# Kernel optimization log

Measured on AMD Instinct MI355X. Metric: run time of the kernel, lower is better.

The kernel has to match this reference:

```python
import jax, jax.numpy as jnp
import numpy as np
import math

B, T, D = 2, 2048, 1024
H, DH = 16, 64          # num_heads, head_dim
DFF = 4096              # 4*d_model
EPS = 1e-5


def _layernorm(x, g, b):
    m = jnp.mean(x, axis=-1, keepdims=True)
    v = jnp.mean(jnp.square(x - m), axis=-1, keepdims=True)
    return (x - m) * jax.lax.rsqrt(v + EPS) * g + b


def setup_inputs() -> dict:
    key = jax.random.key(0)
    ks = jax.random.split(key, 6)
    s = 0.02
    return {
        "x": jax.random.normal(ks[0], (B, T, D), dtype=jnp.float32),
        "ln1_g": jnp.ones((D,), jnp.float32), "ln1_b": jnp.zeros((D,), jnp.float32),
        "ln2_g": jnp.ones((D,), jnp.float32), "ln2_b": jnp.zeros((D,), jnp.float32),
        "w_qkv": jax.random.normal(ks[1], (3 * D, D), jnp.float32) * s,
        "b_qkv": jnp.zeros((3 * D,), jnp.float32),
        "w_out": jax.random.normal(ks[2], (D, D), jnp.float32) * s,
        "b_out": jnp.zeros((D,), jnp.float32),
        "w1": jax.random.normal(ks[3], (DFF, D), jnp.float32) * s,
        "b1": jnp.zeros((DFF,), jnp.float32),
        "w2": jax.random.normal(ks[4], (D, DFF), jnp.float32) * s,
        "b2": jnp.zeros((D,), jnp.float32),
    }


def reference(x, ln1_g, ln1_b, ln2_g, ln2_b, w_qkv, b_qkv, w_out, b_out, w1, b1, w2, b2):
    # --- attention sublayer (Pre-LN) ---
    h = _layernorm(x, ln1_g, ln1_b)                       # [B,T,D]
    qkv = h @ w_qkv.T + b_qkv                             # [B,T,3D]
    qkv = qkv.reshape(B, T, 3, H, DH).transpose(2, 0, 3, 1, 4)  # [3,B,H,T,DH]
    q, k, v = qkv[0], qkv[1], qkv[2]
    scores = jnp.einsum('bhqd,bhkd->bhqk', q, k) / math.sqrt(DH)  # [B,H,T,T]
    causal = jnp.tril(jnp.ones((T, T), dtype=bool))
    scores = jnp.where(causal, scores, -jnp.inf)
    weights = jax.nn.softmax(scores, axis=-1)
    attn = jnp.einsum('bhqk,bhkd->bhqd', weights, v)      # [B,H,T,DH]
    attn = attn.transpose(0, 2, 1, 3).reshape(B, T, D)
    x = x + (attn @ w_out.T + b_out)

    # --- FFN sublayer (Pre-LN, exact GELU) ---
    h2 = _layernorm(x, ln2_g, ln2_b)
    ff = jax.nn.gelu(h2 @ w1.T + b1, approximate=False) @ w2.T + b2
    return x + ff
```

## Files before the change

kernel.cpp:

```cpp
#include <hip/hip_runtime.h>
#include <hip/hip_bf16.h>
#include <cmath>

typedef __bf16 bf16x8 __attribute__((ext_vector_type(8)));
typedef float  f32x4  __attribute__((ext_vector_type(4)));

#define LDS_AS __attribute__((address_space(3)))
#define GLB_AS __attribute__((address_space(1)))

__device__ __forceinline__ void gll16(const void* g, void* l) {
    __builtin_amdgcn_global_load_lds((const GLB_AS unsigned int*)g,
                                     (LDS_AS unsigned int*)l, 16, 0, 0);
}

__device__ __forceinline__ f32x4 mfma16(bf16x8 a, bf16x8 b, f32x4 c) {
    return __builtin_amdgcn_mfma_f32_16x16x32_bf16(a, b, c, 0, 0, 0);
}

__device__ __forceinline__ unsigned short f2bf(float f) {
    __hip_bfloat16 b = __float2bfloat16(f);
    return *reinterpret_cast<unsigned short*>(&b);
}

__device__ __forceinline__ bf16x8 swzfrag(const __hip_bfloat16* __restrict__ lds,
                                          int row, int cb)
{
    const int addr = row * 128 + (cb ^ ((row & 7) << 4));
    return *(const bf16x8*)((const char*)lds + addr);
}

__device__ __forceinline__ void stage64x128B(const char* __restrict__ base, int pitch,
                                             char* __restrict__ lds, int t)
{
#pragma unroll
    for (int i = 0; i < 2; ++i) {
        const int d   = i * 4096 + t * 16;
        const int row = d >> 7;
        const int x   = d & 127;
        const int gx  = x ^ ((row & 7) << 4);
        gll16(base + (size_t)row * pitch + gx, lds + d);
    }
}

__device__ __forceinline__ void stage128x128B(const char* __restrict__ base, int pitch,
                                              char* __restrict__ lds, int t)
{
#pragma unroll
    for (int i = 0; i < 4; ++i) {
        const int d   = i * 4096 + t * 16;
        const int row = d >> 7;
        const int x   = d & 127;
        const int gx  = x ^ ((row & 7) << 4);
        gll16(base + (size_t)row * pitch + gx, lds + d);
    }
}

#define TB   2
#define TT   2048
#define TD   1024
#define TH   16
#define TDH  64
#define TDFF 4096
#define TM   4096

__global__ __launch_bounds__(256)
void cvt_kernel(const float* __restrict__ src, __hip_bfloat16* __restrict__ dst, int n4)
{
    int i = blockIdx.x * 256 + threadIdx.x;
    if (i >= n4) return;
    float4 v = ((const float4*)src)[i];
    ushort4 o;
    o.x = f2bf(v.x); o.y = f2bf(v.y); o.z = f2bf(v.z); o.w = f2bf(v.w);
    ((ushort4*)dst)[i] = o;
}

__global__ __launch_bounds__(256)
void ln_kernel(const float* __restrict__ x, const float* __restrict__ g,
               const float* __restrict__ b, __hip_bfloat16* __restrict__ out)
{
    const int row = blockIdx.x;
    const int t = threadIdx.x;
    const float4 v = *(const float4*)(x + (size_t)row * TD + t * 4);
    float s  = v.x + v.y + v.z + v.w;
    float ss = v.x*v.x + v.y*v.y + v.z*v.z + v.w*v.w;
#pragma unroll
    for (int d = 1; d < 64; d <<= 1) { s += __shfl_xor(s, d); ss += __shfl_xor(ss, d); }
    __shared__ float red[8];
    const int wv = t >> 6, lane = t & 63;
    if (lane == 0) { red[wv] = s; red[4 + wv] = ss; }
    __syncthreads();
    s  = red[0] + red[1] + red[2] + red[3];
    ss = red[4] + red[5] + red[6] + red[7];
    const float mean = s * (1.0f / TD);
    const float var  = ss * (1.0f / TD) - mean * mean;
    const float rstd = rsqrtf(var + 1e-5f);
    const float4 gv = *(const float4*)(g + t * 4);
    const float4 bv = *(const float4*)(b + t * 4);
    ushort4 o;
    o.x = f2bf((v.x - mean) * rstd * gv.x + bv.x);
    o.y = f2bf((v.y - mean) * rstd * gv.y + bv.y);
    o.z = f2bf((v.z - mean) * rstd * gv.z + bv.z);
    o.w = f2bf((v.w - mean) * rstd * gv.w + bv.w);
    *(ushort4*)(out + (size_t)row * TD + t * 4) = o;
}

template<int EPI>
__global__ __launch_bounds__(256)
void gemm_bt(const __hip_bfloat16* __restrict__ A, const __hip_bfloat16* __restrict__ Bw,
             const float* __restrict__ bias, const float* __restrict__ resid,
             float* __restrict__ outf, __hip_bfloat16* __restrict__ outb,
             __hip_bfloat16* __restrict__ qb, __hip_bfloat16* __restrict__ kb,
             __hip_bfloat16* __restrict__ vtb,
             int M, int N, int K)
{
    __shared__ __hip_bfloat16 ldsA[2][128 * 64];
    __shared__ __hip_bfloat16 ldsB[2][128 * 64];
    const int t = threadIdx.x;
    const int lane = t & 63, wv = t >> 6;
    const int wr = wv >> 1, wc = wv & 1;
    const int l15 = lane & 15, lg = lane >> 4;
    const int bn = blockIdx.x, bm = blockIdx.y;
    f32x4 acc[4][4] = {};

    const char* Ab = (const char*)(A  + (size_t)bm * 128 * K);
    const char* Bb = (const char*)(Bw + (size_t)bn * 128 * K);
    const int pitch = K * 2;

    const int nt = K >> 6;
    stage128x128B(Ab, pitch, (char*)ldsA[0], t);
    stage128x128B(Bb, pitch, (char*)ldsB[0], t);
    __syncthreads();

    int cur = 0;
    for (int it = 0; it < nt; ++it) {
        if (it + 1 < nt) {
            const size_t koff = (size_t)(it + 1) * 128;
            stage128x128B(Ab + koff, pitch, (char*)ldsA[cur ^ 1], t);
            stage128x128B(Bb + koff, pitch, (char*)ldsB[cur ^ 1], t);
        }
        bf16x8 af[4][2], bfr[4][2];
#pragma unroll
        for (int mf = 0; mf < 4; ++mf)
#pragma unroll
            for (int kk = 0; kk < 2; ++kk)
                af[mf][kk] = swzfrag(ldsA[cur], wr * 64 + mf * 16 + l15, kk * 64 + lg * 16);
#pragma unroll
        for (int nf = 0; nf < 4; ++nf)
#pragma unroll
            for (int kk = 0; kk < 2; ++kk)
                bfr[nf][kk] = swzfrag(ldsB[cur], wc * 64 + nf * 16 + l15, kk * 64 + lg * 16);
        __builtin_amdgcn_s_setprio(1);
#pragma unroll
        for (int mf = 0; mf < 4; ++mf)
#pragma unroll
            for (int nf = 0; nf < 4; ++nf) {
                acc[mf][nf] = mfma16(af[mf][0], bfr[nf][0], acc[mf][nf]);
                acc[mf][nf] = mfma16(af[mf][1], bfr[nf][1], acc[mf][nf]);
            }
        __builtin_amdgcn_s_setprio(0);
        __syncthreads();
        cur ^= 1;
    }

#pragma unroll
    for (int mf = 0; mf < 4; ++mf) {
#pragma unroll
        for (int nf = 0; nf < 4; ++nf) {
#pragma unroll
            for (int r = 0; r < 4; ++r) {
                const int mg = bm * 128 + wr * 64 + mf * 16 + lg * 4 + r;
                const int ng = bn * 128 + wc * 64 + nf * 16 + l15;
                float v = acc[mf][nf][r] + bias[ng];
                if constexpr (EPI == 1) {
                    const size_t o = (size_t)mg * N + ng;
                    outf[o] = v + resid[o];
                } else if constexpr (EPI == 2) {
                    const float ge = 0.5f * v * (1.0f + erff(v * 0.70710678118654752f));
                    outb[(size_t)mg * N + ng] = __float2bfloat16(ge);
                } else {
                    const int which = ng >> 10;
                    const int hh = (ng >> 6) & 15;
                    const int dh = ng & 63;
                    const int bb = mg >> 11;
                    const int tt = mg & 2047;
                    const int bhid = bb * TH + hh;
                    const __hip_bfloat16 bv = __float2bfloat16(v);
                    if (which == 0)      qb[((size_t)bhid * TT + tt) * TDH + dh] = bv;
                    else if (which == 1) kb[((size_t)bhid * TT + tt) * TDH + dh] = bv;
                    else                 vtb[((size_t)bhid * TDH + dh) * TT + tt] = bv;
                }
            }
        }
    }
}

__global__ __launch_bounds__(256)
void flash_kernel(const __hip_bfloat16* __restrict__ q, const __hip_bfloat16* __restrict__ k,
                  const __hip_bfloat16* __restrict__ vt, __hip_bfloat16* __restrict__ attn)
{
    const int L  = blockIdx.y * gridDim.x + blockIdx.x;
    const int cu = L & 255;
    const int s  = L >> 8;
    const int q0 = cu & 31;
    const int qt = (s & 1) ? (31 - q0) : q0;
    const int bh = s * 8 + (cu >> 5);

    const int t = threadIdx.x;
    const int w = t >> 6, lane = t & 63;
    const int l15 = lane & 15, lg = lane >> 4;
    const int qrow0 = qt * 64 + w * 16;
    const __hip_bfloat16* Qb = q  + (size_t)bh * TT * TDH;
    const __hip_bfloat16* Kb = k  + (size_t)bh * TT * TDH;
    const __hip_bfloat16* Vb = vt + (size_t)bh * TDH * TT;

    __shared__ __hip_bfloat16 kt[2][64 * 64];
    __shared__ __hip_bfloat16 vtt[2][64 * 64];
    __shared__ __hip_bfloat16 plds[4][16 * 64];

    bf16x8 qa[2];
#pragma unroll
    for (int c = 0; c < 2; ++c)
        qa[c] = *(const bf16x8*)(Qb + (size_t)(qrow0 + l15) * TDH + c * 32 + lg * 8);

    f32x4 o[4] = {};
    float mrun = -INFINITY, lrun = 0.0f;

    const int nt = qt + 1;
    int cur = 0;
    stage64x128B((const char*)Kb, 128, (char*)kt[0], t);
    stage64x128B((const char*)Vb, TT * 2, (char*)vtt[0], t);
    __syncthreads();

    for (int it = 0; it < nt; ++it) {
        const int kv0 = it * 64;
        if (it + 1 < nt) {
            stage64x128B((const char*)Kb + (size_t)(kv0 + 64) * 128, 128, (char*)kt[cur ^ 1], t);
            stage64x128B((const char*)Vb + (size_t)(kv0 + 64) * 2, TT * 2, (char*)vtt[cur ^ 1], t);
        }
        f32x4 sc[4] = {};
#pragma unroll
        for (int j = 0; j < 4; ++j) {
            const bf16x8 kb0 = swzfrag(kt[cur], j * 16 + l15, lg * 16);
            const bf16x8 kb1 = swzfrag(kt[cur], j * 16 + l15, 64 + lg * 16);
            sc[j] = mfma16(kb0, qa[0], sc[j]);
            sc[j] = mfma16(kb1, qa[1], sc[j]);
        }
        if (it == nt - 1) {
            const int qg = qrow0 + l15;
#pragma unroll
            for (int j = 0; j < 4; ++j)
#pragma unroll
                for (int r = 0; r < 4; ++r) {
                    const int kvg = kv0 + j * 16 + lg * 4 + r;
                    sc[j][r] = (kvg <= qg) ? sc[j][r] * 0.125f : -INFINITY;
                }
        } else {
#pragma unroll
            for (int j = 0; j < 4; ++j)
#pragma unroll
                for (int r = 0; r < 4; ++r) sc[j][r] *= 0.125f;
        }
        float pm;
        {
            float m0 = fmaxf(fmaxf(sc[0][0], sc[0][1]), fmaxf(sc[0][2], sc[0][3]));
            float m1 = fmaxf(fmaxf(sc[1][0], sc[1][1]), fmaxf(sc[1][2], sc[1][3]));
            float m2 = fmaxf(fmaxf(sc[2][0], sc[2][1]), fmaxf(sc[2][2], sc[2][3]));
            float m3 = fmaxf(fmaxf(sc[3][0], sc[3][1]), fmaxf(sc[3][2], sc[3][3]));
            pm = fmaxf(fmaxf(m0, m1), fmaxf(m2, m3));
        }
        pm = fmaxf(pm, __shfl_xor(pm, 16));
        pm = fmaxf(pm, __shfl_xor(pm, 32));

        const float mn = fmaxf(mrun, pm);
        const float alpha = __expf(mrun - mn);
        mrun = mn;
        f32x4 p[4];
        float rs = 0.0f;
#pragma unroll
        for (int j = 0; j < 4; ++j) {
            float a = 0.0f;
#pragma unroll
            for (int r = 0; r < 4; ++r) { p[j][r] = __expf(sc[j][r] - mn); a += p[j][r]; }
            rs += a;
        }
        rs += __shfl_xor(rs, 16);
        rs += __shfl_xor(rs, 32);
        lrun = lrun * alpha + rs;
#pragma unroll
        for (int nf = 0; nf < 4; ++nf)
#pragma unroll
            for (int r = 0; r < 4; ++r) o[nf][r] *= alpha;
        {
            __hip_bfloat16* pw = plds[w];
#pragma unroll
            for (int j = 0; j < 4; ++j) {
                ushort4 pk;
                pk.x = f2bf(p[j][0]); pk.y = f2bf(p[j][1]);
                pk.z = f2bf(p[j][2]); pk.w = f2bf(p[j][3]);
                const int cb = j * 32 + lg * 8;
                *(ushort4*)((char*)pw + l15 * 128 + (cb ^ ((l15 & 7) << 4))) = pk;
            }
        }
        asm volatile("s_waitcnt lgkmcnt(0)" ::: "memory");
        __builtin_amdgcn_sched_barrier(0);
        bf16x8 pb[2];
#pragma unroll
        for (int c = 0; c < 2; ++c)
            pb[c] = swzfrag(plds[w], l15, c * 64 + lg * 16);
#pragma unroll
        for (int nf = 0; nf < 4; ++nf) {
            const bf16x8 vb0 = swzfrag(vtt[cur], nf * 16 + l15, lg * 16);
            const bf16x8 vb1 = swzfrag(vtt[cur], nf * 16 + l15, 64 + lg * 16);
            o[nf] = mfma16(vb0, pb[0], o[nf]);
            o[nf] = mfma16(vb1, pb[1], o[nf]);
        }
        __syncthreads();
        cur ^= 1;
    }

    const int bb = bh >> 4, hh = bh & 15;
    const float inv = 1.0f / lrun;
    const int tt = qrow0 + l15;
#pragma unroll
    for (int nf = 0; nf < 4; ++nf) {
        const int d0 = nf * 16 + lg * 4;
        ushort4 st;
        st.x = f2bf(o[nf][0] * inv);
        st.y = f2bf(o[nf][1] * inv);
        st.z = f2bf(o[nf][2] * inv);
        st.w = f2bf(o[nf][3] * inv);
        *(ushort4*)(attn + ((size_t)(bb * TT + tt)) * TD + hh * TDH + d0) = st;
    }
}

extern "C" void kernel_launch(void* const* d_in, const int* in_sizes, int n_in,
                              void* d_out, int out_size, void* d_ws, size_t ws_size,
                              hipStream_t stream)
{
    const float* x     = (const float*)d_in[0];
    const float* ln1_g = (const float*)d_in[1];
    const float* ln1_b = (const float*)d_in[2];
    const float* ln2_g = (const float*)d_in[3];
    const float* ln2_b = (const float*)d_in[4];
    const float* w_qkv = (const float*)d_in[5];
    const float* b_qkv = (const float*)d_in[6];
    const float* w_out = (const float*)d_in[7];
    const float* b_out = (const float*)d_in[8];
    const float* w1    = (const float*)d_in[9];
    const float* b1    = (const float*)d_in[10];
    const float* w2    = (const float*)d_in[11];
    const float* b2    = (const float*)d_in[12];

    char* ws = (char*)d_ws;
    __hip_bfloat16* wqkv_bf = (__hip_bfloat16*)(ws + 0);
    __hip_bfloat16* wout_bf = (__hip_bfloat16*)(ws + 6291456);
    __hip_bfloat16* w1_bf   = (__hip_bfloat16*)(ws + 8388608);
    __hip_bfloat16* w2_bf   = (__hip_bfloat16*)(ws + 16777216);
    float*          x2      = (float*)(ws + 25165824);
    __hip_bfloat16* hbuf    = (__hip_bfloat16*)(ws + 41943040);
    __hip_bfloat16* qbuf    = (__hip_bfloat16*)(ws + 50331648);
    __hip_bfloat16* kbuf    = (__hip_bfloat16*)(ws + 58720256);
    __hip_bfloat16* vtbuf   = (__hip_bfloat16*)(ws + 67108864);
    __hip_bfloat16* attnbuf = (__hip_bfloat16*)(ws + 75497472);
    __hip_bfloat16* ff1     = (__hip_bfloat16*)(ws + 50331648);

    cvt_kernel<<<3072, 256, 0, stream>>>(w_qkv, wqkv_bf, 3 * TD * TD / 4);
    cvt_kernel<<<1024, 256, 0, stream>>>(w_out, wout_bf, TD * TD / 4);
    cvt_kernel<<<4096, 256, 0, stream>>>(w1, w1_bf, TDFF * TD / 4);
    cvt_kernel<<<4096, 256, 0, stream>>>(w2, w2_bf, TD * TDFF / 4);

    ln_kernel<<<TM, 256, 0, stream>>>(x, ln1_g, ln1_b, hbuf);
    gemm_bt<0><<<dim3(24, 32), 256, 0, stream>>>(hbuf, wqkv_bf, b_qkv, nullptr,
                                                 nullptr, nullptr, qbuf, kbuf, vtbuf,
                                                 TM, 3 * TD, TD);
    flash_kernel<<<dim3(32, 32), 256, 0, stream>>>(qbuf, kbuf, vtbuf, attnbuf);
    gemm_bt<1><<<dim3(8, 32), 256, 0, stream>>>(attnbuf, wout_bf, b_out, x,
                                                x2, nullptr, nullptr, nullptr, nullptr,
                                                TM, TD, TD);
    ln_kernel<<<TM, 256, 0, stream>>>(x2, ln2_g, ln2_b, hbuf);
    gemm_bt<2><<<dim3(32, 32), 256, 0, stream>>>(hbuf, w1_bf, b1, nullptr,
                                                 nullptr, ff1, nullptr, nullptr, nullptr,
                                                 TM, TDFF, TD);
    gemm_bt<1><<<dim3(8, 32), 256, 0, stream>>>(ff1, w2_bf, b2, x2,
                                                (float*)d_out, nullptr, nullptr, nullptr, nullptr,
                                                TM, TD, TDFF);
}
```

Before: 292.6 us.

## Use split-K with atomic accumulation for output and FFN-down projections

The two GEMMs with N=1024 are split four ways along K, and each split accumulates its partial product into the fp32 output with atomicAdd. A separate kernel first writes residual plus bias into the output buffer. This raises the block count from 256 to 1024 so more compute units stay busy. In exchange it adds atomic read-modify-write traffic, an extra elementwise pass, and a nondeterministic summation order.

```diff
diff --git a/kernel.cpp b/kernel.cpp
--- a/kernel.cpp
+++ b/kernel.cpp
@@ -72,6 +72,19 @@
     ushort4 o;
     o.x = f2bf(v.x); o.y = f2bf(v.y); o.z = f2bf(v.z); o.w = f2bf(v.w);
     ((ushort4*)dst)[i] = o;
+}
+
+__global__ __launch_bounds__(256)
+void addbias_kernel(const float* __restrict__ resid, const float* __restrict__ bias,
+                    float* __restrict__ out)
+{
+    const int row = blockIdx.x;
+    const int t = threadIdx.x;
+    const float4 r = *(const float4*)(resid + (size_t)row * TD + t * 4);
+    const float4 b = *(const float4*)(bias + t * 4);
+    float4 o;
+    o.x = r.x + b.x; o.y = r.y + b.y; o.z = r.z + b.z; o.w = r.w + b.w;
+    *(float4*)(out + (size_t)row * TD + t * 4) = o;
 }
 
 __global__ __launch_bounds__(256)
@@ -111,7 +124,7 @@
              float* __restrict__ outf, __hip_bfloat16* __restrict__ outb,
              __hip_bfloat16* __restrict__ qb, __hip_bfloat16* __restrict__ kb,
              __hip_bfloat16* __restrict__ vtb,
-             int M, int N, int K)
+             int M, int N, int K, int Kpitch)
 {
     __shared__ __hip_bfloat16 ldsA[2][128 * 64];
     __shared__ __hip_bfloat16 ldsB[2][128 * 64];
@@ -119,12 +132,12 @@
     const int lane = t & 63, wv = t >> 6;
     const int wr = wv >> 1, wc = wv & 1;
     const int l15 = lane & 15, lg = lane >> 4;
-    const int bn = blockIdx.x, bm = blockIdx.y;
+    const int bn = blockIdx.x, bm = blockIdx.y, kz = blockIdx.z;
     f32x4 acc[4][4] = {};
 
-    const char* Ab = (const char*)(A  + (size_t)bm * 128 * K);
-    const char* Bb = (const char*)(Bw + (size_t)bn * 128 * K);
-    const int pitch = K * 2;
+    const char* Ab = (const char*)(A  + (size_t)bm * 128 * Kpitch) + (size_t)kz * K * 2;
+    const char* Bb = (const char*)(Bw + (size_t)bn * 128 * Kpitch) + (size_t)kz * K * 2;
+    const int pitch = Kpitch * 2;
 
     const int nt = K >> 6;
     stage128x128B(Ab, pitch, (char*)ldsA[0], t);
@@ -170,24 +183,28 @@
             for (int r = 0; r < 4; ++r) {
                 const int mg = bm * 128 + wr * 64 + mf * 16 + lg * 4 + r;
                 const int ng = bn * 128 + wc * 64 + nf * 16 + l15;
-                float v = acc[mf][nf][r] + bias[ng];
-                if constexpr (EPI == 1) {
-                    const size_t o = (size_t)mg * N + ng;
-                    outf[o] = v + resid[o];
-                } else if constexpr (EPI == 2) {
-                    const float ge = 0.5f * v * (1.0f + erff(v * 0.70710678118654752f));
-                    outb[(size_t)mg * N + ng] = __float2bfloat16(ge);
+                if constexpr (EPI == 3) {
+                    atomicAdd(outf + (size_t)mg * N + ng, acc[mf][nf][r]);
                 } else {
-                    const int which = ng >> 10;
-                    const int hh = (ng >> 6) & 15;
-                    const int dh = ng & 63;
-                    const int bb = mg >> 11;
-                    const int tt = mg & 2047;
-                    const int bhid = bb * TH + hh;
-                    const __hip_bfloat16 bv = __float2bfloat16(v);
-                    if (which == 0)      qb[((size_t)bhid * TT + tt) * TDH + dh] = bv;
-                    else if (which == 1) kb[((size_t)bhid * TT + tt) * TDH + dh] = bv;
-                    else                 vtb[((size_t)bhid * TDH + dh) * TT + tt] = bv;
+                    float v = acc[mf][nf][r] + bias[ng];
+                    if constexpr (EPI == 1) {
+                        const size_t o = (size_t)mg * N + ng;
+                        outf[o] = v + resid[o];
+                    } else if constexpr (EPI == 2) {
+                        const float ge = 0.5f * v * (1.0f + erff(v * 0.70710678118654752f));
+                        outb[(size_t)mg * N + ng] = __float2bfloat16(ge);
+                    } else {
+                        const int which = ng >> 10;
+                        const int hh = (ng >> 6) & 15;
+                        const int dh = ng & 63;
+                        const int bb = mg >> 11;
+                        const int tt = mg & 2047;
+                        const int bhid = bb * TH + hh;
+                        const __hip_bfloat16 bv = __float2bfloat16(v);
+                        if (which == 0)      qb[((size_t)bhid * TT + tt) * TDH + dh] = bv;
+                        else if (which == 1) kb[((size_t)bhid * TT + tt) * TDH + dh] = bv;
+                        else                 vtb[((size_t)bhid * TDH + dh) * TT + tt] = bv;
+                    }
                 }
             }
         }
@@ -372,16 +389,18 @@
     ln_kernel<<<TM, 256, 0, stream>>>(x, ln1_g, ln1_b, hbuf);
     gemm_bt<0><<<dim3(24, 32), 256, 0, stream>>>(hbuf, wqkv_bf, b_qkv, nullptr,
                                                  nullptr, nullptr, qbuf, kbuf, vtbuf,
-                                                 TM, 3 * TD, TD);
+                                                 TM, 3 * TD, TD, TD);
     flash_kernel<<<dim3(32, 32), 256, 0, stream>>>(qbuf, kbuf, vtbuf, attnbuf);
-    gemm_bt<1><<<dim3(8, 32), 256, 0, stream>>>(attnbuf, wout_bf, b_out, x,
-                                                x2, nullptr, nullptr, nullptr, nullptr,
-                                                TM, TD, TD);
+    addbias_kernel<<<TM, 256, 0, stream>>>(x, b_out, x2);
+    gemm_bt<3><<<dim3(8, 32, 4), 256, 0, stream>>>(attnbuf, wout_bf, b_out, nullptr,
+                                                   x2, nullptr, nullptr, nullptr, nullptr,
+                                                   TM, TD, TD / 4, TD);
     ln_kernel<<<TM, 256, 0, stream>>>(x2, ln2_g, ln2_b, hbuf);
     gemm_bt<2><<<dim3(32, 32), 256, 0, stream>>>(hbuf, w1_bf, b1, nullptr,
                                                  nullptr, ff1, nullptr, nullptr, nullptr,
-                                                 TM, TDFF, TD);
-    gemm_bt<1><<<dim3(8, 32), 256, 0, stream>>>(ff1, w2_bf, b2, x2,
-                                                (float*)d_out, nullptr, nullptr, nullptr, nullptr,
-                                                TM, TD, TDFF);
-}
+                                                 TM, TDFF, TD, TD);
+    addbias_kernel<<<TM, 256, 0, stream>>>(x2, b2, (float*)d_out);
+    gemm_bt<3><<<dim3(8, 32, 4), 256, 0, stream>>>(ff1, w2_bf, b2, nullptr,
+                                                   (float*)d_out, nullptr, nullptr, nullptr, nullptr,
+                                                   TM, TD, TDFF / 4, TDFF);
+}
```

Measured after the change: 350.4 us. 19.7% more time.

## Split-K within block for narrow GEMMs and relax pipeline barriers

Applied to the files above, without the earlier changes.

Adds a 512-thread GEMM kernel where two warp groups each process half of K for the same 128x128 tile and reduce through LDS. It is used for the out-projection and FFN down-projection, which launch only 256 blocks. The goal is more waves per CU and better latency hiding on these narrow-N GEMMs. Separately, the main GEMM loop replaces __syncthreads with an explicit vmcnt wait plus s_barrier, so prefetch loads stay in flight past the barrier. The cost is 128KB of LDS per block in the new kernel and a reduction step in its epilogue.

```diff
diff --git a/kernel.cpp b/kernel.cpp
--- a/kernel.cpp
+++ b/kernel.cpp
@@ -120,6 +120,7 @@
     const int wr = wv >> 1, wc = wv & 1;
     const int l15 = lane & 15, lg = lane >> 4;
     const int bn = blockIdx.x, bm = blockIdx.y;
+
     f32x4 acc[4][4] = {};
 
     const char* Ab = (const char*)(A  + (size_t)bm * 128 * K);
@@ -129,7 +130,6 @@
     const int nt = K >> 6;
     stage128x128B(Ab, pitch, (char*)ldsA[0], t);
     stage128x128B(Bb, pitch, (char*)ldsB[0], t);
-    __syncthreads();
 
     int cur = 0;
     for (int it = 0; it < nt; ++it) {
@@ -137,7 +137,12 @@
             const size_t koff = (size_t)(it + 1) * 128;
             stage128x128B(Ab + koff, pitch, (char*)ldsA[cur ^ 1], t);
             stage128x128B(Bb + koff, pitch, (char*)ldsB[cur ^ 1], t);
-        }
+            asm volatile("s_waitcnt vmcnt(8)" ::: "memory");
+        } else {
+            asm volatile("s_waitcnt vmcnt(0)" ::: "memory");
+        }
+        __builtin_amdgcn_s_barrier();
+        __builtin_amdgcn_sched_barrier(0);
         bf16x8 af[4][2], bfr[4][2];
 #pragma unroll
         for (int mf = 0; mf < 4; ++mf)
@@ -158,7 +163,7 @@
                 acc[mf][nf] = mfma16(af[mf][1], bfr[nf][1], acc[mf][nf]);
             }
         __builtin_amdgcn_s_setprio(0);
-        __syncthreads();
+        __builtin_amdgcn_s_barrier();
         cur ^= 1;
     }
 
@@ -194,6 +199,100 @@
     }
 }
 
+__global__ __launch_bounds__(512)
+void gemm_bt_sk(const __hip_bfloat16* __restrict__ A, const __hip_bfloat16* __restrict__ Bw,
+                const float* __restrict__ bias, const float* __restrict__ resid,
+                float* __restrict__ outf, int M, int N, int K)
+{
+    __shared__ char ldsraw[131072];
+    const int t = threadIdx.x;
+    const int tl = t & 255;
+    const int lane = t & 63, w = t >> 6;
+    const int grp = w >> 2;
+    const int wl = w & 3;
+    const int wr = wl >> 1, wc = wl & 1;
+    const int l15 = lane & 15, lg = lane >> 4;
+    const int bn = blockIdx.x, bm = blockIdx.y;
+
+    f32x4 acc[4][4] = {};
+
+    const int Kh = K >> 1;
+    const char* Ab = (const char*)(A  + (size_t)bm * 128 * K) + (size_t)grp * Kh * 2;
+    const char* Bb = (const char*)(Bw + (size_t)bn * 128 * K) + (size_t)grp * Kh * 2;
+    const int pitch = K * 2;
+    char* base = ldsraw + grp * 65536;
+
+    const int nt = Kh >> 6;
+    stage128x128B(Ab, pitch, base, tl);
+    stage128x128B(Bb, pitch, base + 32768, tl);
+
+    for (int it = 0; it < nt; ++it) {
+        const int cb = (it & 1) * 16384;
+        if (it + 1 < nt) {
+            const size_t koff = (size_t)(it + 1) * 128;
+            const int nb = ((it + 1) & 1) * 16384;
+            stage128x128B(Ab + koff, pitch, base + nb, tl);
+            stage128x128B(Bb + koff, pitch, base + 32768 + nb, tl);
+            asm volatile("s_waitcnt vmcnt(8)" ::: "memory");
+        } else {
+            asm volatile("s_waitcnt vmcnt(0)" ::: "memory");
+        }
+        __builtin_amdgcn_s_barrier();
+        __builtin_amdgcn_sched_barrier(0);
+        const __hip_bfloat16* bufA = (const __hip_bfloat16*)(base + cb);
+        const __hip_bfloat16* bufB = (const __hip_bfloat16*)(base + 32768 + cb);
+        bf16x8 af[4][2], bfr[4][2];
+#pragma unroll
+        for (int mf = 0; mf < 4; ++mf)
+#pragma unroll
+            for (int kk = 0; kk < 2; ++kk)
+                af[mf][kk] = swzfrag(bufA, wr * 64 + mf * 16 + l15, kk * 64 + lg * 16);
+#pragma unroll
+        for (int nf = 0; nf < 4; ++nf)
+#pragma unroll
+            for (int kk = 0; kk < 2; ++kk)
+                bfr[nf][kk] = swzfrag(bufB, wc * 64 + nf * 16 + l15, kk * 64 + lg * 16);
+        __builtin_amdgcn_s_setprio(1);
+#pragma unroll
+        for (int mf = 0; mf < 4; ++mf)
+#pragma unroll
+            for (int nf = 0; nf < 4; ++nf) {
+                acc[mf][nf] = mfma16(af[mf][0], bfr[nf][0], acc[mf][nf]);
+                acc[mf][nf] = mfma16(af[mf][1], bfr[nf][1], acc[mf][nf]);
+            }
+        __builtin_amdgcn_s_setprio(0);
+        __builtin_amdgcn_s_barrier();
+    }
+
+    float* xch = (float*)ldsraw;
+    if (grp == 1) {
+#pragma unroll
+        for (int mf = 0; mf < 4; ++mf)
+#pragma unroll
+            for (int nf = 0; nf < 4; ++nf)
+#pragma unroll
+                for (int r = 0; r < 4; ++r)
+                    xch[(wr * 64 + mf * 16 + lg * 4 + r) * 132 + wc * 64 + nf * 16 + l15] =
+                        acc[mf][nf][r];
+    }
+    __syncthreads();
+    if (grp == 0) {
+#pragma unroll
+        for (int mf = 0; mf < 4; ++mf)
+#pragma unroll
+            for (int nf = 0; nf < 4; ++nf)
+#pragma unroll
+                for (int r = 0; r < 4; ++r) {
+                    const int mgl = wr * 64 + mf * 16 + lg * 4 + r;
+                    const int ngl = wc * 64 + nf * 16 + l15;
+                    const int mg = bm * 128 + mgl;
+                    const int ng = bn * 128 + ngl;
+                    const size_t o = (size_t)mg * N + ng;
+                    outf[o] = acc[mf][nf][r] + xch[mgl * 132 + ngl] + bias[ng] + resid[o];
+                }
+    }
+}
+
 __global__ __launch_bounds__(256)
 void flash_kernel(const __hip_bfloat16* __restrict__ q, const __hip_bfloat16* __restrict__ k,
                   const __hip_bfloat16* __restrict__ vt, __hip_bfloat16* __restrict__ attn)
@@ -374,14 +473,12 @@
                                                  nullptr, nullptr, qbuf, kbuf, vtbuf,
                                                  TM, 3 * TD, TD);
     flash_kernel<<<dim3(32, 32), 256, 0, stream>>>(qbuf, kbuf, vtbuf, attnbuf);
-    gemm_bt<1><<<dim3(8, 32), 256, 0, stream>>>(attnbuf, wout_bf, b_out, x,
-                                                x2, nullptr, nullptr, nullptr, nullptr,
-                                                TM, TD, TD);
+    gemm_bt_sk<<<dim3(8, 32), 512, 0, stream>>>(attnbuf, wout_bf, b_out, x,
+                                                x2, TM, TD, TD);
     ln_kernel<<<TM, 256, 0, stream>>>(x2, ln2_g, ln2_b, hbuf);
     gemm_bt<2><<<dim3(32, 32), 256, 0, stream>>>(hbuf, w1_bf, b1, nullptr,
                                                  nullptr, ff1, nullptr, nullptr, nullptr,
                                                  TM, TDFF, TD);
-    gemm_bt<1><<<dim3(8, 32), 256, 0, stream>>>(ff1, w2_bf, b2, x2,
-                                                (float*)d_out, nullptr, nullptr, nullptr, nullptr,
-                                                TM, TD, TDFF);
-}
+    gemm_bt_sk<<<dim3(8, 32), 512, 0, stream>>>(ff1, w2_bf, b2, x2,
+                                                (float*)d_out, TM, TD, TDFF);
+}
```

Result: faster. 253.0 us (-13.5%).

## Split GEMM K dimension across two warp groups within each block

Applied to the files above, without the earlier changes.

The GEMM kernel now launches 512 threads per block. Two groups of four waves each handle half of K with their own double-buffered LDS region (128KB total), and the partial accumulators are reduced through LDS before the epilogue. Barriers are replaced by explicit vmcnt waits plus s_barrier. This doubles the waves per output tile to hide memory latency, especially for the small-grid N=1024 GEMMs. In exchange it uses 128KB of LDS, which limits occupancy to one block per CU, and adds a reduction step.

```diff
diff --git a/kernel.cpp b/kernel.cpp
--- a/kernel.cpp
+++ b/kernel.cpp
@@ -105,50 +105,62 @@
 }
 
 template<int EPI>
-__global__ __launch_bounds__(256)
-void gemm_bt(const __hip_bfloat16* __restrict__ A, const __hip_bfloat16* __restrict__ Bw,
+__global__ __launch_bounds__(512)
+void gemm_sk(const __hip_bfloat16* __restrict__ A, const __hip_bfloat16* __restrict__ Bw,
              const float* __restrict__ bias, const float* __restrict__ resid,
              float* __restrict__ outf, __hip_bfloat16* __restrict__ outb,
              __hip_bfloat16* __restrict__ qb, __hip_bfloat16* __restrict__ kb,
              __hip_bfloat16* __restrict__ vtb,
              int M, int N, int K)
 {
-    __shared__ __hip_bfloat16 ldsA[2][128 * 64];
-    __shared__ __hip_bfloat16 ldsB[2][128 * 64];
+    __shared__ char ldsraw[131072];
     const int t = threadIdx.x;
-    const int lane = t & 63, wv = t >> 6;
-    const int wr = wv >> 1, wc = wv & 1;
+    const int tl = t & 255;
+    const int lane = t & 63, w = t >> 6;
+    const int grp = w >> 2;
+    const int wl = w & 3;
+    const int wr = wl >> 1, wc = wl & 1;
     const int l15 = lane & 15, lg = lane >> 4;
     const int bn = blockIdx.x, bm = blockIdx.y;
+
     f32x4 acc[4][4] = {};
 
-    const char* Ab = (const char*)(A  + (size_t)bm * 128 * K);
-    const char* Bb = (const char*)(Bw + (size_t)bn * 128 * K);
+    const int Kh = K >> 1;
+    const char* Ab = (const char*)(A  + (size_t)bm * 128 * K) + (size_t)grp * Kh * 2;
+    const char* Bb = (const char*)(Bw + (size_t)bn * 128 * K) + (size_t)grp * Kh * 2;
     const int pitch = K * 2;
-
-    const int nt = K >> 6;
-    stage128x128B(Ab, pitch, (char*)ldsA[0], t);
-    stage128x128B(Bb, pitch, (char*)ldsB[0], t);
-    __syncthreads();
-
-    int cur = 0;
+    char* base = ldsraw + grp * 65536;
+
+    const int nt = Kh >> 6;
+    stage128x128B(Ab, pitch, base, tl);
+    stage128x128B(Bb, pitch, base + 32768, tl);
+
     for (int it = 0; it < nt; ++it) {
+        const int cb = (it & 1) * 16384;
         if (it + 1 < nt) {
             const size_t koff = (size_t)(it + 1) * 128;
-            stage128x128B(Ab + koff, pitch, (char*)ldsA[cur ^ 1], t);
-            stage128x128B(Bb + koff, pitch, (char*)ldsB[cur ^ 1], t);
-        }
+            const int nb = ((it + 1) & 1) * 16384;
+            stage128x128B(Ab + koff, pitch, base + nb, tl);
+            stage128x128B(Bb + koff, pitch, base + 32768 + nb, tl);
+            asm volatile("s_waitcnt vmcnt(8)" ::: "memory");
+        } else {
+            asm volatile("s_waitcnt vmcnt(0)" ::: "memory");
+        }
+        __builtin_amdgcn_s_barrier();
+        __builtin_amdgcn_sched_barrier(0);
+        const __hip_bfloat16* bufA = (const __hip_bfloat16*)(base + cb);
+        const __hip_bfloat16* bufB = (const __hip_bfloat16*)(base + 32768 + cb);
         bf16x8 af[4][2], bfr[4][2];
 #pragma unroll
         for (int mf = 0; mf < 4; ++mf)
 #pragma unroll
             for (int kk = 0; kk < 2; ++kk)
-                af[mf][kk] = swzfrag(ldsA[cur], wr * 64 + mf * 16 + l15, kk * 64 + lg * 16);
+                af[mf][kk] = swzfrag(bufA, wr * 64 + mf * 16 + l15, kk * 64 + lg * 16);
 #pragma unroll
         for (int nf = 0; nf < 4; ++nf)
 #pragma unroll
             for (int kk = 0; kk < 2; ++kk)
-                bfr[nf][kk] = swzfrag(ldsB[cur], wc * 64 + nf * 16 + l15, kk * 64 + lg * 16);
+                bfr[nf][kk] = swzfrag(bufB, wc * 64 + nf * 16 + l15, kk * 64 + lg * 16);
         __builtin_amdgcn_s_setprio(1);
 #pragma unroll
         for (int mf = 0; mf < 4; ++mf)
@@ -158,39 +170,52 @@
                 acc[mf][nf] = mfma16(af[mf][1], bfr[nf][1], acc[mf][nf]);
             }
         __builtin_amdgcn_s_setprio(0);
-        __syncthreads();
-        cur ^= 1;
-    }
-
-#pragma unroll
-    for (int mf = 0; mf < 4; ++mf) {
-#pragma unroll
-        for (int nf = 0; nf < 4; ++nf) {
-#pragma unroll
-            for (int r = 0; r < 4; ++r) {
-                const int mg = bm * 128 + wr * 64 + mf * 16 + lg * 4 + r;
-                const int ng = bn * 128 + wc * 64 + nf * 16 + l15;
-                float v = acc[mf][nf][r] + bias[ng];
-                if constexpr (EPI == 1) {
-                    const size_t o = (size_t)mg * N + ng;
-                    outf[o] = v + resid[o];
-                } else if constexpr (EPI == 2) {
-                    const float ge = 0.5f * v * (1.0f + erff(v * 0.70710678118654752f));
-                    outb[(size_t)mg * N + ng] = __float2bfloat16(ge);
-                } else {
-                    const int which = ng >> 10;
-                    const int hh = (ng >> 6) & 15;
-                    const int dh = ng & 63;
-                    const int bb = mg >> 11;
-                    const int tt = mg & 2047;
-                    const int bhid = bb * TH + hh;
-                    const __hip_bfloat16 bv = __float2bfloat16(v);
-                    if (which == 0)      qb[((size_t)bhid * TT + tt) * TDH + dh] = bv;
-                    else if (which == 1) kb[((size_t)bhid * TT + tt) * TDH + dh] = bv;
-                    else                 vtb[((size_t)bhid * TDH + dh) * TT + tt] = bv;
+        __builtin_amdgcn_s_barrier();
+    }
+
+    float* xch = (float*)ldsraw;
+    if (grp == 1) {
+#pragma unroll
+        for (int mf = 0; mf < 4; ++mf)
+#pragma unroll
+            for (int nf = 0; nf < 4; ++nf)
+#pragma unroll
+                for (int r = 0; r < 4; ++r)
+                    xch[(wr * 64 + mf * 16 + lg * 4 + r) * 132 + wc * 64 + nf * 16 + l15] =
+                        acc[mf][nf][r];
+    }
+    __syncthreads();
+    if (grp == 0) {
+#pragma unroll
+        for (int mf = 0; mf < 4; ++mf)
+#pragma unroll
+            for (int nf = 0; nf < 4; ++nf)
+#pragma unroll
+                for (int r = 0; r < 4; ++r) {
+                    const int mgl = wr * 64 + mf * 16 + lg * 4 + r;
+                    const int ngl = wc * 64 + nf * 16 + l15;
+                    const int mg = bm * 128 + mgl;
+                    const int ng = bn * 128 + ngl;
+                    const float v = acc[mf][nf][r] + xch[mgl * 132 + ngl] + bias[ng];
+                    if constexpr (EPI == 1) {
+                        const size_t o = (size_t)mg * N + ng;
+                        outf[o] = v + resid[o];
+                    } else if constexpr (EPI == 2) {
+                        const float ge = 0.5f * v * (1.0f + erff(v * 0.70710678118654752f));
+                        outb[(size_t)mg * N + ng] = __float2bfloat16(ge);
+                    } else {
+                        const int which = ng >> 10;
+                        const int hh = (ng >> 6) & 15;
+                        const int dh = ng & 63;
+                        const int bb = mg >> 11;
+                        const int tt = mg & 2047;
+                        const int bhid = bb * TH + hh;
+                        const __hip_bfloat16 bv = __float2bfloat16(v);
+                        if (which == 0)      qb[((size_t)bhid * TT + tt) * TDH + dh] = bv;
+                        else if (which == 1) kb[((size_t)bhid * TT + tt) * TDH + dh] = bv;
+                        else                 vtb[((size_t)bhid * TDH + dh) * TT + tt] = bv;
+                    }
                 }
-            }
-        }
     }
 }
 
@@ -370,18 +395,18 @@
     cvt_kernel<<<4096, 256, 0, stream>>>(w2, w2_bf, TD * TDFF / 4);
 
     ln_kernel<<<TM, 256, 0, stream>>>(x, ln1_g, ln1_b, hbuf);
-    gemm_bt<0><<<dim3(24, 32), 256, 0, stream>>>(hbuf, wqkv_bf, b_qkv, nullptr,
+    gemm_sk<0><<<dim3(24, 32), 512, 0, stream>>>(hbuf, wqkv_bf, b_qkv, nullptr,
                                                  nullptr, nullptr, qbuf, kbuf, vtbuf,
                                                  TM, 3 * TD, TD);
     flash_kernel<<<dim3(32, 32), 256, 0, stream>>>(qbuf, kbuf, vtbuf, attnbuf);
-    gemm_bt<1><<<dim3(8, 32), 256, 0, stream>>>(attnbuf, wout_bf, b_out, x,
+    gemm_sk<1><<<dim3(8, 32), 512, 0, stream>>>(attnbuf, wout_bf, b_out, x,
                                                 x2, nullptr, nullptr, nullptr, nullptr,
                                                 TM, TD, TD);
     ln_kernel<<<TM, 256, 0, stream>>>(x2, ln2_g, ln2_b, hbuf);
-    gemm_bt<2><<<dim3(32, 32), 256, 0, stream>>>(hbuf, w1_bf, b1, nullptr,
+    gemm_sk<2><<<dim3(32, 32), 512, 0, stream>>>(hbuf, w1_bf, b1, nullptr,
                                                  nullptr, ff1, nullptr, nullptr, nullptr,
                                                  TM, TDFF, TD);
-    gemm_bt<1><<<dim3(8, 32), 256, 0, stream>>>(ff1, w2_bf, b2, x2,
+    gemm_sk<1><<<dim3(8, 32), 512, 0, stream>>>(ff1, w2_bf, b2, x2,
                                                 (float*)d_out, nullptr, nullptr, nullptr, nullptr,
                                                 TM, TD, TDFF);
 }
```

New measurement: 280.4 us. 4.2% less time.
